# Optimization experiments

Measured on AMD Instinct MI355X. Metric: run time of the kernel, lower is better.

Reference implementation:

```python
import jax, jax.numpy as jnp
import numpy as np

NUM_NODES = 50000
NUM_HYPEREDGES = 50000
NNZ = 800000
IN_CH, HID_CH, OUT_CH = 512, 256, 64


def setup_inputs() -> dict:
    key = jax.random.key(0)
    k = jax.random.split(key, 6)
    x = jax.random.normal(k[0], (NUM_NODES, IN_CH), dtype=jnp.float32)
    node_idx = jax.random.randint(k[1], (NNZ,), 0, NUM_NODES)
    hedge_idx = jax.random.randint(k[2], (NNZ,), 0, NUM_HYPEREDGES)
    edge_index = jnp.stack([node_idx, hedge_idx]).astype(jnp.int64)
    W1 = jax.random.normal(k[3], (IN_CH, HID_CH), dtype=jnp.float32) * (1.0 / np.sqrt(IN_CH))
    b1 = jnp.zeros((HID_CH,), dtype=jnp.float32)
    W2 = jax.random.normal(k[4], (HID_CH, OUT_CH), dtype=jnp.float32) * (1.0 / np.sqrt(HID_CH))
    b2 = jnp.zeros((OUT_CH,), dtype=jnp.float32)
    return {"x": x, "edge_index": edge_index, "W1": W1, "b1": b1, "W2": W2, "b2": b2}


def hypergraph_conv(x, node_idx, hedge_idx, W, b):
    # x' = D^{-1} H B^{-1} H^T (x Theta) + b   (PyG HypergraphConv, unit edge weights)
    h = x @ W                                   # [N, F_out]
    ones = jnp.ones(node_idx.shape[0], dtype=x.dtype)
    D = jax.ops.segment_sum(ones, node_idx, num_segments=NUM_NODES)        # node degree
    B = jax.ops.segment_sum(ones, hedge_idx, num_segments=NUM_HYPEREDGES)  # hyperedge degree
    D_inv = jnp.where(D > 0, 1.0 / D, 0.0)
    B_inv = jnp.where(B > 0, 1.0 / B, 0.0)
    # node -> hyperedge aggregation
    m = jax.ops.segment_sum(h[node_idx], hedge_idx, num_segments=NUM_HYPEREDGES)
    m = m * B_inv[:, None]                      # [E, F_out]
    # hyperedge -> node aggregation
    out = jax.ops.segment_sum(m[hedge_idx], node_idx, num_segments=NUM_NODES)
    out = out * D_inv[:, None]                  # [N, F_out]
    return out + b


def reference(x, edge_index, W1, b1, W2, b2):
    node_idx = edge_index[0]
    hedge_idx = edge_index[1]
    h = hypergraph_conv(x, node_idx, hedge_idx, W1, b1)
    h = jax.nn.relu(h)
    h = hypergraph_conv(h, node_idx, hedge_idx, W2, b2)
    return jax.nn.log_softmax(h, axis=1)
```

## Files before the change

### kernel.cpp

```cpp
#include <hip/hip_runtime.h>
#include <math.h>

#define N_NODES  50000
#define N_HEDGES 50000
#define NNZ_     800000
#define IN_CH    512
#define HID_CH   256
#define OUT_CH   64
#define M_PAD    50048
#define NBK      391

#define CVT_BLK  25000
#define BH_BLK   98
#define PK1_BLK  512
#define PK2_BLK  64

typedef __attribute__((ext_vector_type(8))) short bf16x8;
typedef __attribute__((ext_vector_type(4))) float f32x4;

__device__ __forceinline__ unsigned short f2bf(float f) {
    union { float f; unsigned u; } v; v.f = f;
    unsigned r = v.u + 0x7FFFu + ((v.u >> 16) & 1u);
    return (unsigned short)(r >> 16);
}
__device__ __forceinline__ float bf2f(unsigned short u) {
    union { unsigned u; float f; } v; v.u = (unsigned)u << 16; return v.f;
}

#define GLL16(g, l)                                                            \
    __builtin_amdgcn_global_load_lds(                                          \
        (const __attribute__((address_space(1))) void*)(g),                    \
        (__attribute__((address_space(3))) void*)(l), 16, 0, 0)

__global__ void prep_kernel(const float* __restrict__ x, unsigned short* __restrict__ x_bf,
                            const float* __restrict__ W1, unsigned short* __restrict__ Wp1,
                            const float* __restrict__ W2, unsigned short* __restrict__ Wp2,
                            const int* __restrict__ ni, const int* __restrict__ hi,
                            int* __restrict__ bcntN, int* __restrict__ bcntH) {
    const int blk = blockIdx.x;
    const int t = threadIdx.x;
    if (blk < CVT_BLK) {
        const long i = (long)blk * 256 + t;
        const float4 v = *(const float4*)(x + i * 4);
        ushort4 o;
        o.x = f2bf(v.x); o.y = f2bf(v.y); o.z = f2bf(v.z); o.w = f2bf(v.w);
        *(ushort4*)(x_bf + i * 4) = o;
    } else if (blk < CVT_BLK + BH_BLK) {
        __shared__ int lh[NBK], ln[NBK];
        for (int k = t; k < NBK; k += 256) { lh[k] = 0; ln[k] = 0; }
        __syncthreads();
        const int bb = blk - CVT_BLK;
        for (int i4 = bb * 256 + t; i4 < NNZ_ / 4; i4 += BH_BLK * 256) {
            const int4 nv = *(const int4*)(ni + i4 * 4);
            const int4 hv = *(const int4*)(hi + i4 * 4);
            atomicAdd(&ln[nv.x >> 7], 1); atomicAdd(&ln[nv.y >> 7], 1);
            atomicAdd(&ln[nv.z >> 7], 1); atomicAdd(&ln[nv.w >> 7], 1);
            atomicAdd(&lh[hv.x >> 7], 1); atomicAdd(&lh[hv.y >> 7], 1);
            atomicAdd(&lh[hv.z >> 7], 1); atomicAdd(&lh[hv.w >> 7], 1);
        }
        __syncthreads();
        for (int k = t; k < NBK; k += 256) {
            if (ln[k]) atomicAdd(&bcntN[k], ln[k]);
            if (lh[k]) atomicAdd(&bcntH[k], lh[k]);
        }
    } else if (blk < CVT_BLK + BH_BLK + PK1_BLK) {
        const int i = (blk - (CVT_BLK + BH_BLK)) * 256 + t;
        const int kt = i / (HID_CH * 32);
        const int r  = i % (HID_CH * 32);
        const int n  = r >> 5, kk = r & 31;
        Wp1[i] = f2bf(W1[(size_t)(kt * 32 + kk) * HID_CH + n]);
    } else {
        const int i = (blk - (CVT_BLK + BH_BLK + PK1_BLK)) * 256 + t;
        const int kt = i / (OUT_CH * 32);
        const int r  = i % (OUT_CH * 32);
        const int n  = r >> 5, kk = r & 31;
        Wp2[i] = f2bf(W2[(size_t)(kt * 32 + kk) * OUT_CH + n]);
    }
}

__global__ void scan391_kernel(const int* __restrict__ cA, int* __restrict__ offA,
                               int* __restrict__ curA,
                               const int* __restrict__ cB, int* __restrict__ offB,
                               int* __restrict__ curB) {
    const int* cnt = blockIdx.x ? cB : cA;
    int* off = blockIdx.x ? offB : offA;
    int* cur = blockIdx.x ? curB : curA;
    __shared__ int sbuf[512];
    const int t = threadIdx.x;
    const int v = (t < NBK) ? cnt[t] : 0;
    sbuf[t] = v;
    __syncthreads();
    #pragma unroll
    for (int d = 1; d < 512; d <<= 1) {
        int u = (t >= d) ? sbuf[t - d] : 0;
        __syncthreads();
        sbuf[t] += u;
        __syncthreads();
    }
    if (t < NBK) { off[t] = sbuf[t] - v; cur[t] = sbuf[t] - v; }
    if (t == NBK - 1) off[NBK] = sbuf[t];
}

__global__ void bin_kernel(const int* __restrict__ ni, const int* __restrict__ hi,
                           int* __restrict__ bcurN, int* __restrict__ bcurH,
                           unsigned* __restrict__ recN, unsigned* __restrict__ recH) {
    __shared__ int cH[NBK], cN[NBK], bH[NBK], bN[NBK];
    for (int t = threadIdx.x; t < NBK; t += blockDim.x) { cH[t] = 0; cN[t] = 0; }
    __syncthreads();
    const int gid = blockIdx.x * blockDim.x + threadIdx.x;
    const int i0 = gid * 4;
    int4 nv, hv;
    const bool act = (i0 < NNZ_);
    if (act) {
        nv = *(const int4*)(ni + i0);
        hv = *(const int4*)(hi + i0);
        atomicAdd(&cN[nv.x >> 7], 1); atomicAdd(&cN[nv.y >> 7], 1);
        atomicAdd(&cN[nv.z >> 7], 1); atomicAdd(&cN[nv.w >> 7], 1);
        atomicAdd(&cH[hv.x >> 7], 1); atomicAdd(&cH[hv.y >> 7], 1);
        atomicAdd(&cH[hv.z >> 7], 1); atomicAdd(&cH[hv.w >> 7], 1);
    }
    __syncthreads();
    for (int t = threadIdx.x; t < NBK; t += blockDim.x) {
        bH[t] = cH[t] ? atomicAdd(&bcurH[t], cH[t]) : 0;
        bN[t] = cN[t] ? atomicAdd(&bcurN[t], cN[t]) : 0;
    }
    __syncthreads();
    for (int t = threadIdx.x; t < NBK; t += blockDim.x) { cH[t] = bH[t]; cN[t] = bN[t]; }
    __syncthreads();
    if (act) {
        int nn[4] = {nv.x, nv.y, nv.z, nv.w};
        int hh[4] = {hv.x, hv.y, hv.z, hv.w};
        #pragma unroll
        for (int k = 0; k < 4; ++k) {
            int p = atomicAdd(&cH[hh[k] >> 7], 1);
            recH[p] = ((unsigned)(hh[k] & 127) << 16) | (unsigned)nn[k];
            p = atomicAdd(&cN[nn[k] >> 7], 1);
            recN[p] = ((unsigned)(nn[k] & 127) << 16) | (unsigned)hh[k];
        }
    }
}

__global__ void buildcsr_kernel(const int* __restrict__ bstartH, const unsigned* __restrict__ recH,
                                int* __restrict__ offH, int* __restrict__ colH,
                                float* __restrict__ Binv,
                                const int* __restrict__ bstartN, const unsigned* __restrict__ recN,
                                int* __restrict__ offN, int* __restrict__ colN,
                                float* __restrict__ Dinv) {
    int b = blockIdx.x;
    const int* bstart; const unsigned* rec; int* off; int* col; float* inv;
    if (b < NBK) { bstart = bstartH; rec = recH; off = offH; col = colH; inv = Binv; }
    else { b -= NBK; bstart = bstartN; rec = recN; off = offN; col = colN; inv = Dinv; }
    const int s = bstart[b], e = bstart[b + 1];
    const int t = threadIdx.x;
    __shared__ int lc[128], ps[128], cur[128];
    if (t < 128) lc[t] = 0;
    __syncthreads();
    for (int i = s + t; i < e; i += 256) atomicAdd(&lc[rec[i] >> 16], 1);
    __syncthreads();
    if (t < 128) ps[t] = lc[t];
    __syncthreads();
    #pragma unroll
    for (int d = 1; d < 128; d <<= 1) {
        int v = (t >= d && t < 128) ? ps[t - d] : 0;
        __syncthreads();
        if (t < 128) ps[t] += v;
        __syncthreads();
    }
    if (t < 128) {
        const int excl = s + ps[t] - lc[t];
        cur[t] = excl;
        const int id = b * 128 + t;
        if (id < N_NODES) {
            off[id] = excl;
            inv[id] = lc[t] > 0 ? 1.f / (float)lc[t] : 0.f;
        }
    }
    if (b == NBK - 1 && t == 255) off[N_NODES] = bstart[NBK];
    __syncthreads();
    for (int i = s + t; i < e; i += 256) {
        const unsigned r = rec[i];
        const int p = atomicAdd(&cur[r >> 16], 1);
        col[p] = (int)(r & 0xFFFFu);
    }
}

template <int BN>
__global__ void mfma_gemm_kernel(const unsigned short* __restrict__ A,
                                 const unsigned short* __restrict__ Wp,
                                 unsigned short* __restrict__ C, int M, int N, int K) {
    constexpr int NT = BN / 32;
    __shared__ unsigned short As[128 * 32];
    __shared__ unsigned short Bs[BN * 32];

    const int tid  = threadIdx.x;
    const int wave = tid >> 6;
    const int lane = tid & 63;
    const int wr = wave >> 1;
    const int wc = wave & 1;
    const int quad = lane >> 4;
    const int l15  = lane & 15;
    const int row0 = blockIdx.y * 128;
    const int col0 = blockIdx.x * BN;

    const size_t a_g0   = (size_t)(row0 + wave * 16 + (lane >> 2)) * K + (lane & 3) * 8;
    const int    a_l0   = (wave * 16 + (lane >> 2)) * 32 + (lane & 3) * 8;
    const size_t b_gbase = ((size_t)col0 + wave * 16 + (lane >> 2)) * 32 + (lane & 3) * 8;
    const int    b_l0   = (wave * 16 + (lane >> 2)) * 32 + (lane & 3) * 8;

    f32x4 acc[4][NT];
    #pragma unroll
    for (int mt = 0; mt < 4; ++mt)
        #pragma unroll
        for (int nt = 0; nt < NT; ++nt)
            acc[mt][nt] = (f32x4)0.f;

    const int KT = K / 32;
    for (int kt = 0; kt < KT; ++kt) {
        __syncthreads();
        GLL16(A + a_g0 + (size_t)kt * 32, As + a_l0);
        GLL16(A + a_g0 + (size_t)(kt * 32) + (size_t)64 * K, As + a_l0 + 64 * 32);
        const size_t bk = (size_t)kt * N * 32;
        GLL16(Wp + bk + b_gbase, Bs + b_l0);
        if (BN == 128)
            GLL16(Wp + bk + b_gbase + 64 * 32, Bs + b_l0 + 64 * 32);
        __syncthreads();

        bf16x8 af[4], bf[NT];
        #pragma unroll
        for (int mt = 0; mt < 4; ++mt)
            af[mt] = *(const bf16x8*)(As + (wr * 64 + mt * 16 + l15) * 32 + quad * 8);
        #pragma unroll
        for (int nt = 0; nt < NT; ++nt)
            bf[nt] = *(const bf16x8*)(Bs + (wc * (BN / 2) + nt * 16 + l15) * 32 + quad * 8);
        #pragma unroll
        for (int mt = 0; mt < 4; ++mt)
            #pragma unroll
            for (int nt = 0; nt < NT; ++nt)
                acc[mt][nt] = __builtin_amdgcn_mfma_f32_16x16x32_bf16(
                    af[mt], bf[nt], acc[mt][nt], 0, 0, 0);
    }

    #pragma unroll
    for (int mt = 0; mt < 4; ++mt) {
        const int gr0 = row0 + wr * 64 + mt * 16 + quad * 4;
        #pragma unroll
        for (int nt = 0; nt < NT; ++nt) {
            const int gc = col0 + wc * (BN / 2) + nt * 16 + l15;
            #pragma unroll
            for (int r = 0; r < 4; ++r) {
                int gr = gr0 + r;
                if (gr < M) C[(size_t)gr * N + gc] = f2bf(acc[mt][nt][r]);
            }
        }
    }
}

template <bool EPI>
__global__ void gather256_kernel(const unsigned short* __restrict__ src,
                                 unsigned short* __restrict__ dst,
                                 const int* __restrict__ off, const int* __restrict__ col,
                                 const float* __restrict__ scale,
                                 const float* __restrict__ bias, int nrows) {
    int row = blockIdx.x * (blockDim.x >> 6) + (threadIdx.x >> 6);
    if (row >= nrows) return;
    int lane = threadIdx.x & 63;
    int s = off[row], e = off[row + 1];
    float ax = 0.f, ay = 0.f, az = 0.f, aw = 0.f;
    int j = s;
    for (; j + 3 < e; j += 4) {
        const ushort4 u0 = *(const ushort4*)(src + (size_t)col[j]     * HID_CH + (lane << 2));
        const ushort4 u1 = *(const ushort4*)(src + (size_t)col[j + 1] * HID_CH + (lane << 2));
        const ushort4 u2 = *(const ushort4*)(src + (size_t)col[j + 2] * HID_CH + (lane << 2));
        const ushort4 u3 = *(const ushort4*)(src + (size_t)col[j + 3] * HID_CH + (lane << 2));
        ax += (bf2f(u0.x) + bf2f(u1.x)) + (bf2f(u2.x) + bf2f(u3.x));
        ay += (bf2f(u0.y) + bf2f(u1.y)) + (bf2f(u2.y) + bf2f(u3.y));
        az += (bf2f(u0.z) + bf2f(u1.z)) + (bf2f(u2.z) + bf2f(u3.z));
        aw += (bf2f(u0.w) + bf2f(u1.w)) + (bf2f(u2.w) + bf2f(u3.w));
    }
    for (; j < e; ++j) {
        const ushort4 u = *(const ushort4*)(src + (size_t)col[j] * HID_CH + (lane << 2));
        ax += bf2f(u.x); ay += bf2f(u.y); az += bf2f(u.z); aw += bf2f(u.w);
    }
    float sc = scale[row];
    float rx = ax * sc, ry = ay * sc, rz = az * sc, rw = aw * sc;
    if (EPI) {
        const float4 b = *(const float4*)(bias + (lane << 2));
        rx = fmaxf(rx + b.x, 0.f); ry = fmaxf(ry + b.y, 0.f);
        rz = fmaxf(rz + b.z, 0.f); rw = fmaxf(rw + b.w, 0.f);
    }
    ushort4 o;
    o.x = f2bf(rx); o.y = f2bf(ry); o.z = f2bf(rz); o.w = f2bf(rw);
    *(ushort4*)(dst + (size_t)row * HID_CH + (lane << 2)) = o;
}

template <bool LSM>
__global__ void gather64_kernel(const unsigned short* __restrict__ src, void* __restrict__ dstv,
                                const int* __restrict__ off, const int* __restrict__ col,
                                const float* __restrict__ scale,
                                const float* __restrict__ bias, int nrows) {
    int row = blockIdx.x * (blockDim.x >> 6) + (threadIdx.x >> 6);
    if (row >= nrows) return;
    int lane = threadIdx.x & 63;
    int s = off[row], e = off[row + 1];
    float acc = 0.f;
    int j = s;
    for (; j + 3 < e; j += 4) {
        const float v0 = bf2f(src[(size_t)col[j]     * OUT_CH + lane]);
        const float v1 = bf2f(src[(size_t)col[j + 1] * OUT_CH + lane]);
        const float v2 = bf2f(src[(size_t)col[j + 2] * OUT_CH + lane]);
        const float v3 = bf2f(src[(size_t)col[j + 3] * OUT_CH + lane]);
        acc += (v0 + v1) + (v2 + v3);
    }
    for (; j < e; ++j) acc += bf2f(src[(size_t)col[j] * OUT_CH + lane]);
    float v = acc * scale[row];
    if (LSM) {
        v += bias[lane];
        float m = v;
        #pragma unroll
        for (int o = 32; o >= 1; o >>= 1) m = fmaxf(m, __shfl_xor(m, o));
        float ex = expf(v - m);
        float su = ex;
        #pragma unroll
        for (int o = 32; o >= 1; o >>= 1) su += __shfl_xor(su, o);
        ((float*)dstv)[(size_t)row * OUT_CH + lane] = v - m - logf(su);
    } else {
        ((unsigned short*)dstv)[(size_t)row * OUT_CH + lane] = f2bf(v);
    }
}

extern "C" void kernel_launch(void* const* d_in, const int* in_sizes, int n_in,
                              void* d_out, int out_size, void* d_ws, size_t ws_size,
                              hipStream_t stream) {
    const float* x  = (const float*)d_in[0];
    const int*   ei = (const int*)d_in[1];
    const float* W1 = (const float*)d_in[2];
    const float* b1 = (const float*)d_in[3];
    const float* W2 = (const float*)d_in[4];
    const float* b2 = (const float*)d_in[5];
    float* out = (float*)d_out;

    const int* node_idx  = ei;
    const int* hedge_idx = ei + NNZ_;

    const size_t RCAP = (size_t)M_PAD * IN_CH / 2;
    float* regionA = (float*)d_ws;
    float* regionB = regionA + RCAP;
    float* Dinv = regionB + RCAP;
    float* Binv = Dinv + N_NODES;
    int* offN = (int*)(Binv + N_HEDGES);
    int* offH = offN + N_NODES + 1;
    int* colN = offH + N_HEDGES + 1;
    int* colH = colN + NNZ_;
    unsigned short* Wp1 = (unsigned short*)(colH + NNZ_);
    unsigned short* Wp2 = Wp1 + IN_CH * HID_CH;
    int* bcntH   = (int*)(Wp2 + HID_CH * OUT_CH);
    int* bcntN   = bcntH + 400;
    int* bstartH = bcntN + 400;
    int* bstartN = bstartH + 400;
    int* bcurH   = bstartN + 400;
    int* bcurN   = bcurH + 400;

    unsigned* recH = (unsigned*)regionA;
    unsigned* recN = recH + NNZ_;

    unsigned short* x_bf  = (unsigned short*)regionB;
    unsigned short* h1_bf = (unsigned short*)regionA;
    unsigned short* m1_bf = (unsigned short*)regionB;
    unsigned short* h2_bf = (unsigned short*)regionA;
    unsigned short* g_bf  = (unsigned short*)regionB;
    unsigned short* m2_bf = (unsigned short*)regionB + (size_t)M_PAD * OUT_CH;

    hipMemsetAsync(bcntH, 0, 800 * sizeof(int), stream);
    prep_kernel<<<CVT_BLK + BH_BLK + PK1_BLK + PK2_BLK, 256, 0, stream>>>(
        x, x_bf, W1, Wp1, W2, Wp2, node_idx, hedge_idx, bcntN, bcntH);
    scan391_kernel<<<2, 512, 0, stream>>>(bcntH, bstartH, bcurH, bcntN, bstartN, bcurN);
    bin_kernel<<<200, 1024, 0, stream>>>(node_idx, hedge_idx, bcurN, bcurH, recN, recH);
    buildcsr_kernel<<<2 * NBK, 256, 0, stream>>>(bstartH, recH, offH, colH, Binv,
                                                 bstartN, recN, offN, colN, Dinv);

    mfma_gemm_kernel<128><<<dim3(HID_CH / 128, (N_NODES + 127) / 128), 256, 0, stream>>>(
        x_bf, Wp1, h1_bf, N_NODES, HID_CH, IN_CH);
    gather256_kernel<false><<<(N_HEDGES + 3) / 4, 256, 0, stream>>>(
        h1_bf, m1_bf, offH, colH, Binv, nullptr, N_HEDGES);
    gather256_kernel<true><<<(N_NODES + 3) / 4, 256, 0, stream>>>(
        m1_bf, h2_bf, offN, colN, Dinv, b1, N_NODES);

    mfma_gemm_kernel<64><<<dim3(OUT_CH / 64, (N_NODES + 127) / 128), 256, 0, stream>>>(
        h2_bf, Wp2, g_bf, N_NODES, OUT_CH, HID_CH);
    gather64_kernel<false><<<(N_HEDGES + 3) / 4, 256, 0, stream>>>(
        g_bf, m2_bf, offH, colH, Binv, nullptr, N_HEDGES);
    gather64_kernel<true><<<(N_NODES + 3) / 4, 256, 0, stream>>>(
        m2_bf, out, offN, colN, Dinv, b2, N_NODES);
}
```

Baseline: 433.2 us.

## Store hidden features in 64-column chunks so gathers stay L2-resident

The first GEMM now writes its output as four column chunks of 64 features each, laid out [chunk][row][64]. The 256-wide gathers are replaced by chunked gathers: each block handles one chunk for four rows, and blocks are ordered chunk-major so the random row accesses for a chunk hit a smaller ~6.4MB working set that can fit in cache. The gather loops are also unrolled to 8 loads in flight. In exchange, each lane loads 2 bytes instead of 8, so per-wave requests are narrower. The col/off index arrays are also re-read once per chunk, four times in total.

```diff
diff --git a/kernel.cpp b/kernel.cpp
--- a/kernel.cpp
+++ b/kernel.cpp
@@ -9,6 +9,7 @@
 #define OUT_CH   64
 #define M_PAD    50048
 #define NBK      391
+#define BPC      12500
 
 #define CVT_BLK  25000
 #define BH_BLK   98
@@ -184,7 +185,7 @@
     }
 }
 
-template <int BN>
+template <int BN, bool CHUNK>
 __global__ void mfma_gemm_kernel(const unsigned short* __restrict__ A,
                                  const unsigned short* __restrict__ Wp,
                                  unsigned short* __restrict__ C, int M, int N, int K) {
@@ -245,52 +246,53 @@
         const int gr0 = row0 + wr * 64 + mt * 16 + quad * 4;
         #pragma unroll
         for (int nt = 0; nt < NT; ++nt) {
-            const int gc = col0 + wc * (BN / 2) + nt * 16 + l15;
             #pragma unroll
             for (int r = 0; r < 4; ++r) {
                 int gr = gr0 + r;
-                if (gr < M) C[(size_t)gr * N + gc] = f2bf(acc[mt][nt][r]);
+                if (CHUNK) {
+                    const size_t base = (size_t)(col0 / 64 + wc) * ((size_t)M_PAD * 64);
+                    C[base + (size_t)gr * 64 + nt * 16 + l15] = f2bf(acc[mt][nt][r]);
+                } else {
+                    const int gc = col0 + wc * (BN / 2) + nt * 16 + l15;
+                    if (gr < M) C[(size_t)gr * N + gc] = f2bf(acc[mt][nt][r]);
+                }
             }
         }
     }
 }
 
 template <bool EPI>
-__global__ void gather256_kernel(const unsigned short* __restrict__ src,
-                                 unsigned short* __restrict__ dst,
-                                 const int* __restrict__ off, const int* __restrict__ col,
-                                 const float* __restrict__ scale,
-                                 const float* __restrict__ bias, int nrows) {
-    int row = blockIdx.x * (blockDim.x >> 6) + (threadIdx.x >> 6);
-    if (row >= nrows) return;
-    int lane = threadIdx.x & 63;
+__global__ void gather256c_kernel(const unsigned short* __restrict__ src,
+                                  unsigned short* __restrict__ dst,
+                                  const int* __restrict__ off, const int* __restrict__ col,
+                                  const float* __restrict__ scale,
+                                  const float* __restrict__ bias, int nrows) {
+    const int chunk = blockIdx.x / BPC;
+    const int row = (blockIdx.x % BPC) * 4 + (threadIdx.x >> 6);
+    const int lane = threadIdx.x & 63;
+    const unsigned short* sb = src + (size_t)chunk * ((size_t)M_PAD * 64) + lane;
     int s = off[row], e = off[row + 1];
-    float ax = 0.f, ay = 0.f, az = 0.f, aw = 0.f;
+    float acc = 0.f;
     int j = s;
-    for (; j + 3 < e; j += 4) {
-        const ushort4 u0 = *(const ushort4*)(src + (size_t)col[j]     * HID_CH + (lane << 2));
-        const ushort4 u1 = *(const ushort4*)(src + (size_t)col[j + 1] * HID_CH + (lane << 2));
-        const ushort4 u2 = *(const ushort4*)(src + (size_t)col[j + 2] * HID_CH + (lane << 2));
-        const ushort4 u3 = *(const ushort4*)(src + (size_t)col[j + 3] * HID_CH + (lane << 2));
-        ax += (bf2f(u0.x) + bf2f(u1.x)) + (bf2f(u2.x) + bf2f(u3.x));
-        ay += (bf2f(u0.y) + bf2f(u1.y)) + (bf2f(u2.y) + bf2f(u3.y));
-        az += (bf2f(u0.z) + bf2f(u1.z)) + (bf2f(u2.z) + bf2f(u3.z));
-        aw += (bf2f(u0.w) + bf2f(u1.w)) + (bf2f(u2.w) + bf2f(u3.w));
-    }
-    for (; j < e; ++j) {
-        const ushort4 u = *(const ushort4*)(src + (size_t)col[j] * HID_CH + (lane << 2));
-        ax += bf2f(u.x); ay += bf2f(u.y); az += bf2f(u.z); aw += bf2f(u.w);
-    }
-    float sc = scale[row];
-    float rx = ax * sc, ry = ay * sc, rz = az * sc, rw = aw * sc;
+    for (; j + 7 < e; j += 8) {
+        const float v0 = bf2f(sb[col[j]     << 6]);
+        const float v1 = bf2f(sb[col[j + 1] << 6]);
+        const float v2 = bf2f(sb[col[j + 2] << 6]);
+        const float v3 = bf2f(sb[col[j + 3] << 6]);
+        const float v4 = bf2f(sb[col[j + 4] << 6]);
+        const float v5 = bf2f(sb[col[j + 5] << 6]);
+        const float v6 = bf2f(sb[col[j + 6] << 6]);
+        const float v7 = bf2f(sb[col[j + 7] << 6]);
+        acc += ((v0 + v1) + (v2 + v3)) + ((v4 + v5) + (v6 + v7));
+    }
+    for (; j < e; ++j) acc += bf2f(sb[col[j] << 6]);
+    float r = acc * scale[row];
     if (EPI) {
-        const float4 b = *(const float4*)(bias + (lane << 2));
-        rx = fmaxf(rx + b.x, 0.f); ry = fmaxf(ry + b.y, 0.f);
-        rz = fmaxf(rz + b.z, 0.f); rw = fmaxf(rw + b.w, 0.f);
-    }
-    ushort4 o;
-    o.x = f2bf(rx); o.y = f2bf(ry); o.z = f2bf(rz); o.w = f2bf(rw);
-    *(ushort4*)(dst + (size_t)row * HID_CH + (lane << 2)) = o;
+        r = fmaxf(r + bias[chunk * 64 + lane], 0.f);
+        dst[(size_t)row * HID_CH + chunk * 64 + lane] = f2bf(r);
+    } else {
+        dst[(size_t)chunk * ((size_t)M_PAD * 64) + (size_t)row * 64 + lane] = f2bf(r);
+    }
 }
 
 template <bool LSM>
@@ -304,14 +306,18 @@
     int s = off[row], e = off[row + 1];
     float acc = 0.f;
     int j = s;
-    for (; j + 3 < e; j += 4) {
-        const float v0 = bf2f(src[(size_t)col[j]     * OUT_CH + lane]);
-        const float v1 = bf2f(src[(size_t)col[j + 1] * OUT_CH + lane]);
-        const float v2 = bf2f(src[(size_t)col[j + 2] * OUT_CH + lane]);
-        const float v3 = bf2f(src[(size_t)col[j + 3] * OUT_CH + lane]);
-        acc += (v0 + v1) + (v2 + v3);
-    }
-    for (; j < e; ++j) acc += bf2f(src[(size_t)col[j] * OUT_CH + lane]);
+    for (; j + 7 < e; j += 8) {
+        const float v0 = bf2f(src[((size_t)col[j]     << 6) + lane]);
+        const float v1 = bf2f(src[((size_t)col[j + 1] << 6) + lane]);
+        const float v2 = bf2f(src[((size_t)col[j + 2] << 6) + lane]);
+        const float v3 = bf2f(src[((size_t)col[j + 3] << 6) + lane]);
+        const float v4 = bf2f(src[((size_t)col[j + 4] << 6) + lane]);
+        const float v5 = bf2f(src[((size_t)col[j + 5] << 6) + lane]);
+        const float v6 = bf2f(src[((size_t)col[j + 6] << 6) + lane]);
+        const float v7 = bf2f(src[((size_t)col[j + 7] << 6) + lane]);
+        acc += ((v0 + v1) + (v2 + v3)) + ((v4 + v5) + (v6 + v7));
+    }
+    for (; j < e; ++j) acc += bf2f(src[((size_t)col[j] << 6) + lane]);
     float v = acc * scale[row];
     if (LSM) {
         v += bias[lane];
@@ -364,8 +370,8 @@
     unsigned* recN = recH + NNZ_;
 
     unsigned short* x_bf  = (unsigned short*)regionB;
-    unsigned short* h1_bf = (unsigned short*)regionA;
-    unsigned short* m1_bf = (unsigned short*)regionB;
+    unsigned short* h1c   = (unsigned short*)regionA;
+    unsigned short* m1c   = (unsigned short*)regionB;
     unsigned short* h2_bf = (unsigned short*)regionA;
     unsigned short* g_bf  = (unsigned short*)regionB;
     unsigned short* m2_bf = (unsigned short*)regionB + (size_t)M_PAD * OUT_CH;
@@ -378,14 +384,14 @@
     buildcsr_kernel<<<2 * NBK, 256, 0, stream>>>(bstartH, recH, offH, colH, Binv,
                                                  bstartN, recN, offN, colN, Dinv);
 
-    mfma_gemm_kernel<128><<<dim3(HID_CH / 128, (N_NODES + 127) / 128), 256, 0, stream>>>(
-        x_bf, Wp1, h1_bf, N_NODES, HID_CH, IN_CH);
-    gather256_kernel<false><<<(N_HEDGES + 3) / 4, 256, 0, stream>>>(
-        h1_bf, m1_bf, offH, colH, Binv, nullptr, N_HEDGES);
-    gather256_kernel<true><<<(N_NODES + 3) / 4, 256, 0, stream>>>(
-        m1_bf, h2_bf, offN, colN, Dinv, b1, N_NODES);
-
-    mfma_gemm_kernel<64><<<dim3(OUT_CH / 64, (N_NODES + 127) / 128), 256, 0, stream>>>(
+    mfma_gemm_kernel<128, true><<<dim3(HID_CH / 128, (N_NODES + 127) / 128), 256, 0, stream>>>(
+        x_bf, Wp1, h1c, N_NODES, HID_CH, IN_CH);
+    gather256c_kernel<false><<<4 * BPC, 256, 0, stream>>>(
+        h1c, m1c, offH, colH, Binv, nullptr, N_HEDGES);
+    gather256c_kernel<true><<<4 * BPC, 256, 0, stream>>>(
+        m1c, h2_bf, offN, colN, Dinv, b1, N_NODES);
+
+    mfma_gemm_kernel<64, false><<<dim3(OUT_CH / 64, (N_NODES + 127) / 128), 256, 0, stream>>>(
         h2_bf, Wp2, g_bf, N_NODES, OUT_CH, HID_CH);
     gather64_kernel<false><<<(N_HEDGES + 3) / 4, 256, 0, stream>>>(
         g_bf, m2_bf, offH, colH, Binv, nullptr, N_HEDGES);
```

Measured after the change: 558.9 us. 1.29x slower.
